# Optimization experiments

Measured on AMD Instinct MI355X. Metric: run time of the kernel, lower is better.

The kernel has to match this reference:

```python
import jax, jax.numpy as jnp
import numpy as np

B, T, C, H = 8, 1024, 1024, 8
D = C // H  # head dim

def setup_inputs() -> dict:
    key = jax.random.key(0)
    ks = jax.random.split(key, 6)
    s = 1.0 / np.sqrt(C)
    return {
        "x": jax.random.normal(ks[0], (B, T, C), jnp.float32),
        "mask": jnp.ones((B, T), jnp.int32),
        "Wq": jax.random.normal(ks[1], (C, C), jnp.float32) * s,
        "bq": jnp.zeros((C,), jnp.float32),
        "Wk": jax.random.normal(ks[2], (C, C), jnp.float32) * s,
        "bk": jnp.zeros((C,), jnp.float32),
        "Wv": jax.random.normal(ks[3], (C, C), jnp.float32) * s,
        "bv": jnp.zeros((C,), jnp.float32),
        "Wp": jax.random.normal(ks[4], (C, C), jnp.float32) * s,
        "bp": jnp.zeros((C,), jnp.float32),
    }

def reference(x, mask, Wq, bq, Wk, bk, Wv, bv, Wp, bp):
    # torch Linear: x @ W.T + b
    q = (x @ Wq.T + bq).reshape(B, T, H, D).transpose(0, 2, 1, 3)  # b h t d
    k = (x @ Wk.T + bk).reshape(B, T, H, D).transpose(0, 2, 1, 3)
    v = (x @ Wv.T + bv).reshape(B, T, H, D).transpose(0, 2, 1, 3)
    att = jnp.einsum('bhqd,bhkd->bhqk', q, k) * (1.0 / np.sqrt(D))
    m = mask.astype(jnp.float32)[:, None, None, :]  # (B,1,1,T)
    att = jnp.where(m == 0, -jnp.inf, att)
    att = jax.nn.softmax(att, axis=-1)
    y = jnp.einsum('bhqk,bhkd->bhqd', att, v)
    y = y.transpose(0, 2, 1, 3).reshape(B, T, C)
    return y @ Wp.T + bp
```

## Files before the change

### kernel.cpp

```cpp
#include <hip/hip_runtime.h>

typedef __bf16 bf16;
typedef __attribute__((ext_vector_type(8))) bf16 bf16x8;
typedef __attribute__((ext_vector_type(4))) float f32x4;

#define GLDS16(g, l) __builtin_amdgcn_global_load_lds( \
    (const __attribute__((address_space(1))) void*)(g), \
    (__attribute__((address_space(3))) void*)(l), 16, 0, 0)

#define QSCALE 0.12751744f

static __device__ __forceinline__ f32x4 MFMA(bf16x8 a, bf16x8 b, f32x4 c) {
    return __builtin_amdgcn_mfma_f32_16x16x32_bf16(a, b, c, 0, 0, 0);
}

__global__ __launch_bounds__(256) void convert_kernel(
    const float* __restrict__ x, const float* __restrict__ wq,
    const float* __restrict__ wk, const float* __restrict__ wv,
    const float* __restrict__ wp,
    bf16* __restrict__ xb, bf16* __restrict__ wqkvb, bf16* __restrict__ wpb)
{
    int bid = blockIdx.x;
    const float* src; bf16* dst; int base;
    if (bid < 4096)      { src = x;  dst = xb;              base = bid * 2048; }
    else if (bid < 4608) { src = wq; dst = wqkvb;           base = (bid - 4096) * 2048; }
    else if (bid < 5120) { src = wk; dst = wqkvb + 1048576; base = (bid - 4608) * 2048; }
    else if (bid < 5632) { src = wv; dst = wqkvb + 2097152; base = (bid - 5120) * 2048; }
    else                 { src = wp; dst = wpb;             base = (bid - 5632) * 2048; }
    int i = base + threadIdx.x * 8;
    const f32x4* s4 = (const f32x4*)(src + i);
    f32x4 a = s4[0], c = s4[1];
    bf16x8 v;
    #pragma unroll
    for (int e = 0; e < 4; ++e) { v[e] = (bf16)a[e]; v[e + 4] = (bf16)c[e]; }
    *(bf16x8*)(dst + i) = v;
}

template <int MODE, int NTN>
__global__ __launch_bounds__(128, 2) void gemm2(
    const bf16* __restrict__ A, const bf16* __restrict__ B,
    const float* __restrict__ bias0, const float* __restrict__ bias1,
    const float* __restrict__ bias2,
    bf16* __restrict__ q_out, bf16* __restrict__ k_out, bf16* __restrict__ vt_out,
    float* __restrict__ f_out)
{
    constexpr int K = 1024;
    constexpr int NT = K / 32;
    constexpr int NWG = 64 * NTN;
    const int tid = threadIdx.x;
    const int lane = tid & 63;
    const int wid = tid >> 6;
    const int l15 = lane & 15, l4 = lane >> 4;

    const int g = blockIdx.x;
    const int lin = (g & 7) * (NWG / 8) + (g >> 3);
    const int m0 = (lin / NTN) * 128, n0 = (lin % NTN) * 128;

    __shared__ __align__(16) bf16 lds[2][2][4096];

    const int qq = (tid & 7) ^ ((tid >> 3) & 7);
    const int rb = 2 * (tid >> 3) + (qq >> 2);
    const int cc = qq & 3;
    const bf16* aB = A + (size_t)(m0 + rb) * K + cc * 8;
    const bf16* bB = B + (size_t)(n0 + rb) * K + cc * 8;
    auto stage = [&](int buf, int t) {
        #pragma unroll
        for (int c = 0; c < 4; ++c)
            GLDS16(aB + (size_t)(c * 32) * K + t * 32, &lds[buf][0][c * 1024 + tid * 8]);
        #pragma unroll
        for (int c = 0; c < 4; ++c)
            GLDS16(bB + (size_t)(c * 32) * K + t * 32, &lds[buf][1][c * 1024 + tid * 8]);
    };

    const int physc = (((l15 & 1) * 4 + l4) ^ ((l15 >> 1) & 7)) * 16;
    const int aoff = (wid * 32 + (l15 >> 1)) * 128 + physc;
    const int boff = (l15 >> 1) * 128 + physc;
    #define RA(buf, f) (*(const bf16x8*)((const char*)lds[buf][0] + aoff + (f) * 1024))
    #define RB(buf, j) (*(const bf16x8*)((const char*)lds[buf][1] + boff + (j) * 1024))

    f32x4 acc[4][8];
    #pragma unroll
    for (int f = 0; f < 4; ++f)
        #pragma unroll
        for (int j = 0; j < 8; ++j)
            #pragma unroll
            for (int e = 0; e < 4; ++e) acc[f][j][e] = 0.f;

    stage(0, 0);
    __syncthreads();

    for (int t = 0; t < NT; ++t) {
        const int buf = t & 1;
        if (t + 1 < NT) stage(buf ^ 1, t + 1);
        bf16x8 af[4], bfr[8];
        #pragma unroll
        for (int f = 0; f < 4; ++f) af[f] = RA(buf, f);
        #pragma unroll
        for (int j = 0; j < 8; ++j) bfr[j] = RB(buf, j);
        __builtin_amdgcn_s_setprio(1);
        #pragma unroll
        for (int f = 0; f < 4; ++f)
            #pragma unroll
            for (int j = 0; j < 8; ++j)
                acc[f][j] = MFMA(af[f], bfr[j], acc[f][j]);
        __builtin_amdgcn_s_setprio(0);
        __syncthreads();
    }
    #undef RA
    #undef RB

    #pragma unroll
    for (int f = 0; f < 4; ++f) {
        #pragma unroll
        for (int j = 0; j < 8; ++j) {
            #pragma unroll
            for (int r = 0; r < 4; ++r) {
                int m = m0 + wid * 64 + f * 16 + l4 * 4 + r;
                int n = n0 + j * 16 + l15;
                float v = acc[f][j][r];
                if (MODE == 0) {
                    if (n0 < 1024) {
                        q_out[m * 1024 + n] = (bf16)((v + bias0[n]) * QSCALE);
                    } else if (n0 < 2048) {
                        int nn = n - 1024;
                        k_out[m * 1024 + nn] = (bf16)(v + bias1[nn]);
                    } else {
                        int nn = n - 2048;
                        int hl = nn >> 7, d = nn & 127;
                        int bb = m >> 10, tt = m & 1023;
                        vt_out[((bb * 8 + hl) * 128 + d) * 1024 + tt] = (bf16)(v + bias2[nn]);
                    }
                } else {
                    f_out[m * 1024 + n] = v + bias0[n];
                }
            }
        }
    }
}

__global__ __launch_bounds__(256, 2) void attn_kernel(
    const bf16* __restrict__ qb, const bf16* __restrict__ kb,
    const bf16* __restrict__ vtb, const int* __restrict__ mask,
    bf16* __restrict__ yb)
{
    const int tid = threadIdx.x;
    const int lane = tid & 63;
    const int wid = tid >> 6;
    const int g = blockIdx.x;
    const int orig = (g & 7) * 64 + (g >> 3);
    const int bh = orig >> 3;
    const int qt = orig & 7;
    const int b = bh >> 3;
    const int h = bh & 7;
    const int m0 = b * 1024 + qt * 128;
    const int l15 = lane & 15, l4 = lane >> 4;

    __shared__ __align__(16) char smem[81920];
    auto stageKV = [&](int bufKV, int kt) {
        char* Kb = smem + bufKV * 16384;
        char* Vb = smem + 32768 + bufKV * 16384;
        #pragma unroll
        for (int n = 0; n < 4; ++n)
            GLDS16(kb + (b * 1024 + kt + n * 16 + (tid >> 4)) * 1024 + h * 128 +
                       (((tid & 15) ^ ((tid >> 4) & 7)) * 8),
                   Kb + n * 4096 + tid * 16);
        #pragma unroll
        for (int n = 0; n < 4; ++n)
            GLDS16(vtb + (bh * 128 + n * 32 + (tid >> 3)) * 1024 + kt +
                       (((tid & 7) ^ ((tid >> 3) & 7)) * 8),
                   Vb + n * 4096 + tid * 16);
    };

    bf16x8 qf[2][4];
    #pragma unroll
    for (int i = 0; i < 2; ++i)
        #pragma unroll
        for (int kc = 0; kc < 4; ++kc)
            qf[i][kc] = *(const bf16x8*)(qb +
                (m0 + wid * 32 + i * 16 + l15) * 1024 + h * 128 + kc * 32 + l4 * 8);

    f32x4 o[2][8];
    #pragma unroll
    for (int i = 0; i < 2; ++i)
        #pragma unroll
        for (int jd = 0; jd < 8; ++jd)
            #pragma unroll
            for (int e = 0; e < 4; ++e) o[i][jd][e] = 0.f;
    float l_run[2][4];
    #pragma unroll
    for (int i = 0; i < 2; ++i)
        #pragma unroll
        for (int r = 0; r < 4; ++r) l_run[i][r] = 0.f;

    stageKV(0, 0);
    __syncthreads();

    for (int t = 0; t < 16; ++t) {
        const int buf = t & 1;
        const int kt = t * 64;
        if (t + 1 < 16) stageKV(buf ^ 1, kt + 64);

        int mv[4];
        #pragma unroll
        for (int j = 0; j < 4; ++j)
            mv[j] = mask[b * 1024 + kt + j * 16 + l15];

        const char* Ks = smem + buf * 16384;
        const char* Vs = smem + 32768 + buf * 16384;

        f32x4 s[2][4];
        #pragma unroll
        for (int i = 0; i < 2; ++i)
            #pragma unroll
            for (int j = 0; j < 4; ++j)
                #pragma unroll
                for (int e = 0; e < 4; ++e) s[i][j][e] = 0.f;
        #pragma unroll
        for (int kc = 0; kc < 4; ++kc) {
            bf16x8 kf[4];
            #pragma unroll
            for (int j = 0; j < 4; ++j)
                kf[j] = *(const bf16x8*)(Ks + (j * 16 + l15) * 256 +
                    (((kc * 4 + l4) ^ (lane & 7)) * 16));
            __builtin_amdgcn_s_setprio(1);
            #pragma unroll
            for (int i = 0; i < 2; ++i)
                #pragma unroll
                for (int j = 0; j < 4; ++j)
                    s[i][j] = MFMA(qf[i][kc], kf[j], s[i][j]);
            __builtin_amdgcn_s_setprio(0);
        }

        #pragma unroll
        for (int i = 0; i < 2; ++i)
            #pragma unroll
            for (int j = 0; j < 4; ++j) {
                if (mv[j] == 0) {
                    #pragma unroll
                    for (int e = 0; e < 4; ++e) s[i][j][e] = -1e30f;
                }
                #pragma unroll
                for (int r = 0; r < 4; ++r) {
                    float p = __builtin_amdgcn_exp2f(s[i][j][r]);
                    s[i][j][r] = p;
                    l_run[i][r] += p;
                }
            }

        #pragma unroll
        for (int i = 0; i < 2; ++i)
            #pragma unroll
            for (int j = 0; j < 4; ++j)
                #pragma unroll
                for (int r = 0; r < 4; ++r) {
                    int row = i * 16 + l4 * 4 + r;
                    int col = j * 16 + l15;
                    *(bf16*)(smem + 65536 + wid * 4096 + row * 128 +
                             (((col >> 3) ^ (row & 7)) * 16) + (col & 7) * 2) =
                        (bf16)s[i][j][r];
                }

        #pragma unroll
        for (int k2 = 0; k2 < 2; ++k2) {
            bf16x8 pa[2];
            #pragma unroll
            for (int i = 0; i < 2; ++i)
                pa[i] = *(const bf16x8*)(smem + 65536 + wid * 4096 +
                    (i * 16 + l15) * 128 + (((k2 * 4 + l4) ^ (l15 & 7)) * 16));
            __builtin_amdgcn_s_setprio(1);
            #pragma unroll
            for (int jd = 0; jd < 8; ++jd) {
                bf16x8 vf = *(const bf16x8*)(Vs + (jd * 16 + l15) * 128 +
                    (((k2 * 4 + l4) ^ (l15 & 7)) * 16));
                o[0][jd] = MFMA(pa[0], vf, o[0][jd]);
                o[1][jd] = MFMA(pa[1], vf, o[1][jd]);
            }
            __builtin_amdgcn_s_setprio(0);
        }
        __syncthreads();
    }

    #pragma unroll
    for (int off = 8; off >= 1; off >>= 1)
        #pragma unroll
        for (int i = 0; i < 2; ++i)
            #pragma unroll
            for (int r = 0; r < 4; ++r) l_run[i][r] += __shfl_xor(l_run[i][r], off);
    #pragma unroll
    for (int i = 0; i < 2; ++i) {
        float inv[4];
        #pragma unroll
        for (int r = 0; r < 4; ++r) inv[r] = 1.0f / fmaxf(l_run[i][r], 1e-30f);
        #pragma unroll
        for (int jd = 0; jd < 8; ++jd)
            #pragma unroll
            for (int r = 0; r < 4; ++r)
                yb[(m0 + wid * 32 + i * 16 + l4 * 4 + r) * 1024 +
                   h * 128 + jd * 16 + l15] = (bf16)(o[i][jd][r] * inv[r]);
    }
}

extern "C" void kernel_launch(void* const* d_in, const int* in_sizes, int n_in,
                              void* d_out, int out_size, void* d_ws, size_t ws_size,
                              hipStream_t stream)
{
    (void)in_sizes; (void)n_in; (void)out_size; (void)ws_size;
    const float* x  = (const float*)d_in[0];
    const int* mask = (const int*)d_in[1];
    const float* Wq = (const float*)d_in[2];
    const float* bq = (const float*)d_in[3];
    const float* Wk = (const float*)d_in[4];
    const float* bk = (const float*)d_in[5];
    const float* Wv = (const float*)d_in[6];
    const float* bv = (const float*)d_in[7];
    const float* Wp = (const float*)d_in[8];
    const float* bp = (const float*)d_in[9];
    float* out = (float*)d_out;

    char* ws = (char*)d_ws;
    bf16* xb    = (bf16*)(ws);
    bf16* wqkvb = (bf16*)(ws + (16u << 20));
    bf16* wpb   = (bf16*)(ws + (22u << 20));
    bf16* qbuf  = (bf16*)(ws + (24u << 20));
    bf16* kbuf  = (bf16*)(ws + (40u << 20));
    bf16* vtb   = (bf16*)(ws + (56u << 20));
    bf16* ybuf  = (bf16*)(ws + (72u << 20));

    convert_kernel<<<6144, 256, 0, stream>>>(x, Wq, Wk, Wv, Wp, xb, wqkvb, wpb);
    gemm2<0, 24><<<1536, 128, 0, stream>>>(xb, wqkvb, bq, bk, bv,
                                           qbuf, kbuf, vtb, nullptr);
    attn_kernel<<<512, 256, 0, stream>>>(qbuf, kbuf, vtb, mask, ybuf);
    gemm2<1, 8><<<512, 128, 0, stream>>>(ybuf, wpb, bp, nullptr, nullptr,
                                         nullptr, nullptr, nullptr, out);
}
```

Before: 191.8 us.

## Retile projection GEMMs to 256x128 tiles with 8 waves per block

The GEMM kernel moves from 128-thread blocks computing 128x128 tiles to 512-thread blocks computing 256x128 tiles. The 8 waves sit in a 4x2 grid, each owning a 64x64 sub-tile. Each block stages both A halves and the B tile into shared LDS per K step, so B is reused across twice as many rows and global loads are spread over more threads. Per-wave accumulators shrink from 32 to 16 MFMA tiles, which frees registers for higher occupancy. In exchange each wave gets less MFMA work per LDS read, and a barrier now synchronizes 8 waves.

```diff
diff --git a/kernel.cpp b/kernel.cpp
--- a/kernel.cpp
+++ b/kernel.cpp
@@ -37,7 +37,7 @@
 }
 
 template <int MODE, int NTN>
-__global__ __launch_bounds__(128, 2) void gemm2(
+__global__ __launch_bounds__(512, 4) void gemm2(
     const bf16* __restrict__ A, const bf16* __restrict__ B,
     const float* __restrict__ bias0, const float* __restrict__ bias1,
     const float* __restrict__ bias2,
@@ -46,43 +46,43 @@
 {
     constexpr int K = 1024;
     constexpr int NT = K / 32;
-    constexpr int NWG = 64 * NTN;
+    constexpr int NWG = 32 * NTN;
     const int tid = threadIdx.x;
     const int lane = tid & 63;
     const int wid = tid >> 6;
+    const int wr = wid >> 1;
+    const int wc = wid & 1;
     const int l15 = lane & 15, l4 = lane >> 4;
 
     const int g = blockIdx.x;
     const int lin = (g & 7) * (NWG / 8) + (g >> 3);
-    const int m0 = (lin / NTN) * 128, n0 = (lin % NTN) * 128;
-
-    __shared__ __align__(16) bf16 lds[2][2][4096];
-
-    const int qq = (tid & 7) ^ ((tid >> 3) & 7);
-    const int rb = 2 * (tid >> 3) + (qq >> 2);
+    const int m0 = (lin / NTN) * 256, n0 = (lin % NTN) * 128;
+
+    __shared__ __align__(16) bf16 lds[2][12288];
+
+    const int t3 = tid >> 3, pp = tid & 7;
+    const int qq = pp ^ (t3 & 7);
+    const int rb = 2 * t3 + (qq >> 2);
     const int cc = qq & 3;
     const bf16* aB = A + (size_t)(m0 + rb) * K + cc * 8;
     const bf16* bB = B + (size_t)(n0 + rb) * K + cc * 8;
     auto stage = [&](int buf, int t) {
-        #pragma unroll
-        for (int c = 0; c < 4; ++c)
-            GLDS16(aB + (size_t)(c * 32) * K + t * 32, &lds[buf][0][c * 1024 + tid * 8]);
-        #pragma unroll
-        for (int c = 0; c < 4; ++c)
-            GLDS16(bB + (size_t)(c * 32) * K + t * 32, &lds[buf][1][c * 1024 + tid * 8]);
+        GLDS16(aB + t * 32,                    &lds[buf][tid * 8]);
+        GLDS16(aB + (size_t)128 * K + t * 32,  &lds[buf][4096 + tid * 8]);
+        GLDS16(bB + t * 32,                    &lds[buf][8192 + tid * 8]);
     };
 
     const int physc = (((l15 & 1) * 4 + l4) ^ ((l15 >> 1) & 7)) * 16;
-    const int aoff = (wid * 32 + (l15 >> 1)) * 128 + physc;
-    const int boff = (l15 >> 1) * 128 + physc;
-    #define RA(buf, f) (*(const bf16x8*)((const char*)lds[buf][0] + aoff + (f) * 1024))
-    #define RB(buf, j) (*(const bf16x8*)((const char*)lds[buf][1] + boff + (j) * 1024))
-
-    f32x4 acc[4][8];
+    const int aoff = (wr * 32 + (l15 >> 1)) * 128 + physc;
+    const int boff = 16384 + (wc * 32 + (l15 >> 1)) * 128 + physc;
+    #define RA(buf, f) (*(const bf16x8*)((const char*)lds[buf] + aoff + (f) * 1024))
+    #define RB(buf, j) (*(const bf16x8*)((const char*)lds[buf] + boff + (j) * 1024))
+
+    f32x4 acc[4][4];
     #pragma unroll
     for (int f = 0; f < 4; ++f)
         #pragma unroll
-        for (int j = 0; j < 8; ++j)
+        for (int j = 0; j < 4; ++j)
             #pragma unroll
             for (int e = 0; e < 4; ++e) acc[f][j][e] = 0.f;
 
@@ -92,16 +92,16 @@
     for (int t = 0; t < NT; ++t) {
         const int buf = t & 1;
         if (t + 1 < NT) stage(buf ^ 1, t + 1);
-        bf16x8 af[4], bfr[8];
+        bf16x8 af[4], bfr[4];
         #pragma unroll
         for (int f = 0; f < 4; ++f) af[f] = RA(buf, f);
         #pragma unroll
-        for (int j = 0; j < 8; ++j) bfr[j] = RB(buf, j);
+        for (int j = 0; j < 4; ++j) bfr[j] = RB(buf, j);
         __builtin_amdgcn_s_setprio(1);
         #pragma unroll
         for (int f = 0; f < 4; ++f)
             #pragma unroll
-            for (int j = 0; j < 8; ++j)
+            for (int j = 0; j < 4; ++j)
                 acc[f][j] = MFMA(af[f], bfr[j], acc[f][j]);
         __builtin_amdgcn_s_setprio(0);
         __syncthreads();
@@ -112,11 +112,11 @@
     #pragma unroll
     for (int f = 0; f < 4; ++f) {
         #pragma unroll
-        for (int j = 0; j < 8; ++j) {
+        for (int j = 0; j < 4; ++j) {
             #pragma unroll
             for (int r = 0; r < 4; ++r) {
-                int m = m0 + wid * 64 + f * 16 + l4 * 4 + r;
-                int n = n0 + j * 16 + l15;
+                int m = m0 + wr * 64 + f * 16 + l4 * 4 + r;
+                int n = n0 + wc * 64 + j * 16 + l15;
                 float v = acc[f][j][r];
                 if (MODE == 0) {
                     if (n0 < 1024) {
@@ -327,9 +327,9 @@
     bf16* ybuf  = (bf16*)(ws + (72u << 20));
 
     convert_kernel<<<6144, 256, 0, stream>>>(x, Wq, Wk, Wv, Wp, xb, wqkvb, wpb);
-    gemm2<0, 24><<<1536, 128, 0, stream>>>(xb, wqkvb, bq, bk, bv,
-                                           qbuf, kbuf, vtb, nullptr);
+    gemm2<0, 24><<<768, 512, 0, stream>>>(xb, wqkvb, bq, bk, bv,
+                                          qbuf, kbuf, vtb, nullptr);
     attn_kernel<<<512, 256, 0, stream>>>(qbuf, kbuf, vtb, mask, ybuf);
-    gemm2<1, 8><<<512, 128, 0, stream>>>(ybuf, wpb, bp, nullptr, nullptr,
+    gemm2<1, 8><<<256, 512, 0, stream>>>(ybuf, wpb, bp, nullptr, nullptr,
                                          nullptr, nullptr, nullptr, out);
 }
```

Measured after the change: 176.7 us. 7.9% less time.
